# Performance work log

Hardware: AMD Instinct MI355X
Metric: run time of the kernel (lower is better)

## Reference

```python
import jax, jax.numpy as jnp
import numpy as np

L, B, T, D, H, FF = 4, 8, 1024, 256, 8, 1024
DK = D // H
SCALE = 1.0 / np.sqrt(DK)


def _ln(x, g, b, eps=1e-6):
    m = jnp.mean(x, axis=-1, keepdims=True)
    v = jnp.mean(jnp.square(x - m), axis=-1, keepdims=True)
    return (x - m) * jax.lax.rsqrt(v + eps) * g + b


def _l2norm(x, eps=1e-8):
    n = jnp.sqrt(jnp.sum(jnp.square(x), axis=-1, keepdims=True))
    return x / jnp.maximum(n, eps)


def setup_inputs() -> dict:
    key = jax.random.key(0)
    ks = jax.random.split(key, 8)
    s = 0.02
    inp = {
        'x': jax.random.normal(ks[0], (B, T, D), dtype=jnp.float32),
        'padding_mask': jnp.zeros((B, T), dtype=bool),
        'ln1_g': jnp.ones((L, D), jnp.float32), 'ln1_b': jnp.zeros((L, D), jnp.float32),
        'qn_g': jnp.ones((L, D), jnp.float32), 'qn_b': jnp.zeros((L, D), jnp.float32),
        'Wqkv': jax.random.normal(ks[1], (L, 3 * D, D), jnp.float32) * s,
        'bqkv': jnp.zeros((L, 3 * D), jnp.float32),
        'Wo': jax.random.normal(ks[2], (L, D, D), jnp.float32) * s,
        'bo': jnp.zeros((L, D), jnp.float32),
        'ln2_g': jnp.ones((L, D), jnp.float32), 'ln2_b': jnp.zeros((L, D), jnp.float32),
        'W1': jax.random.normal(ks[3], (L, FF, D), jnp.float32) * s,
        'b1': jnp.zeros((L, FF), jnp.float32),
        'W2': jax.random.normal(ks[4], (L, D, FF), jnp.float32) * s,
        'b2': jnp.zeros((L, D), jnp.float32),
        'alpha': jnp.full((L,), 0.1, jnp.float32),
        'beta': jnp.full((L,), 0.1, jnp.float32),
    }
    return inp


def _block(x, pad_mask, p):
    (g1, bb1, qg, qb, wqkv, bqkv, wo, bo, g2, bb2, w1, b1, w2, b2, a, be) = p
    Bn, Tn, Dn = x.shape
    # --- SemiCausalAttention on norm1(x) ---
    xn = _ln(x, g1, bb1)
    h = _ln(xn, qg, qb)                      # q_norm LayerNorm
    qkv = h @ wqkv.T + bqkv                  # [B,T,3D]
    qkv = qkv.reshape(Bn, Tn, 3, H, DK).transpose(2, 0, 3, 1, 4)  # [3,B,H,T,dk]
    Q, K, V = qkv[0], qkv[1], qkv[2]
    Q = _l2norm(Q)
    K = _l2norm(K)
    scores = jnp.einsum('bhtd,bhsd->bhts', Q, K) * SCALE
    scores = jnp.clip(scores, -10.0, 10.0)
    causal = jnp.triu(jnp.ones((Tn, Tn), dtype=bool), k=1)        # True = future
    scores = jnp.where(causal[None, None], -10000.0, scores)
    scores = jnp.where(pad_mask[:, None, None, :], -10000.0, scores)
    attn = jax.nn.softmax(scores, axis=-1)
    ao = jnp.einsum('bhts,bhsd->bhtd', attn, V)                   # [B,H,T,dk]
    ao = ao.transpose(0, 2, 1, 3).reshape(Bn, Tn, Dn)
    attn_out = (ao @ wo.T + bo) * 0.5
    x = x + jnp.tanh(a) * attn_out
    # --- FFN ---
    f = _ln(x, g2, bb2)
    f = jax.nn.gelu(f @ w1.T + b1, approximate=False)
    f = f @ w2.T + b2
    x = x + jnp.tanh(be) * f
    return jnp.clip(x, -100.0, 100.0)


def reference(x, padding_mask, ln1_g, ln1_b, qn_g, qn_b, Wqkv, bqkv, Wo, bo,
              ln2_g, ln2_b, W1, b1, W2, b2, alpha, beta):
    params = (ln1_g, ln1_b, qn_g, qn_b, Wqkv, bqkv, Wo, bo,
              ln2_g, ln2_b, W1, b1, W2, b2, alpha, beta)

    def step(carry, p):
        return _block(carry, padding_mask, p), None

    out, _ = jax.lax.scan(step, x, params)
    return out
```

## Files before the change

### kernel.cpp

```cpp
#include <hip/hip_runtime.h>
#include <hip/hip_bf16.h>
#include <math.h>

#define BB 8
#define TT 1024
#define DD 256
#define HH 8
#define BT 8192

typedef __attribute__((ext_vector_type(4))) float f32x4;
typedef __attribute__((ext_vector_type(16))) float f32x16;
typedef __attribute__((ext_vector_type(8))) short short8;
typedef __attribute__((ext_vector_type(4))) short short4v;
typedef __attribute__((ext_vector_type(8))) __bf16 bf16x8;

__device__ inline float bf2f(short s) {
  unsigned int u = ((unsigned int)(unsigned short)s) << 16;
  return __builtin_bit_cast(float, u);
}
__device__ inline short f2bf(float f) {
  unsigned int u = __builtin_bit_cast(unsigned int, f);
  unsigned int lsb = (u >> 16) & 1u;
  u += 0x7fffu + lsb;
  return (short)(u >> 16);
}
__device__ inline unsigned int cvtpk(float lo, float hi) {
  unsigned int r;
  asm("v_cvt_pk_bf16_f32 %0, %1, %2" : "=v"(r) : "v"(lo), "v"(hi));
  return r;
}

__device__ inline f32x4 mfma16(short8 a, short8 b, f32x4 c) {
  return __builtin_amdgcn_mfma_f32_16x16x32_bf16(
      __builtin_bit_cast(bf16x8, a), __builtin_bit_cast(bf16x8, b), c, 0, 0, 0);
}
__device__ inline f32x16 mfma32(short8 a, short8 b, f32x16 c) {
  return __builtin_amdgcn_mfma_f32_32x32x16_bf16(
      __builtin_bit_cast(bf16x8, a), __builtin_bit_cast(bf16x8, b), c, 0, 0, 0);
}

__device__ inline void gload_lds16(void* lds, const void* g) {
  __builtin_amdgcn_global_load_lds(
      (const __attribute__((address_space(1))) unsigned int*)g,
      (__attribute__((address_space(3))) unsigned int*)lds, 16, 0, 0);
}

__global__ __launch_bounds__(256) void cvt_all(
    const float4* __restrict__ s0, short4v* __restrict__ d0, int n0,
    const float4* __restrict__ s1, short4v* __restrict__ d1, int n1,
    const float4* __restrict__ s2, short4v* __restrict__ d2, int n2,
    const float4* __restrict__ s3, short4v* __restrict__ d3, int n3)
{
  int i = blockIdx.x * 256 + threadIdx.x;
  const float4* s; short4v* d;
  if (i < n0) { s = s0 + i; d = d0 + i; }
  else if ((i -= n0) < n1) { s = s1 + i; d = d1 + i; }
  else if ((i -= n1) < n2) { s = s2 + i; d = d2 + i; }
  else if ((i -= n2) < n3) { s = s3 + i; d = d3 + i; }
  else return;
  float4 v = *s;
  short4v o;
  o[0] = f2bf(v.x); o[1] = f2bf(v.y); o[2] = f2bf(v.z); o[3] = f2bf(v.w);
  *d = o;
}

__global__ __launch_bounds__(256) void ln_kernel(
    const float* __restrict__ Xin,
    const float* __restrict__ g1, const float* __restrict__ b1,
    const float* __restrict__ g2, const float* __restrict__ b2,
    short* __restrict__ out)
{
  const int row = blockIdx.x * 4 + (threadIdx.x >> 6);
  const int lane = threadIdx.x & 63;
  const float4 v = *(const float4*)(Xin + (size_t)row * 256 + lane * 4);
  float y[4] = {v.x, v.y, v.z, v.w};

  float s = y[0] + y[1] + y[2] + y[3];
  #pragma unroll
  for (int m = 32; m >= 1; m >>= 1) s += __shfl_xor(s, m, 64);
  float mean = s * (1.0f / 256.0f);
  float sq = 0.f;
  #pragma unroll
  for (int i = 0; i < 4; ++i) { y[i] -= mean; sq += y[i] * y[i]; }
  #pragma unroll
  for (int m = 32; m >= 1; m >>= 1) sq += __shfl_xor(sq, m, 64);
  float rs = rsqrtf(sq * (1.0f / 256.0f) + 1e-6f);
  #pragma unroll
  for (int i = 0; i < 4; ++i) y[i] = y[i] * rs * g1[lane * 4 + i] + b1[lane * 4 + i];

  float s2 = y[0] + y[1] + y[2] + y[3];
  #pragma unroll
  for (int m = 32; m >= 1; m >>= 1) s2 += __shfl_xor(s2, m, 64);
  float m2 = s2 * (1.0f / 256.0f);
  float sq2 = 0.f;
  #pragma unroll
  for (int i = 0; i < 4; ++i) { y[i] -= m2; sq2 += y[i] * y[i]; }
  #pragma unroll
  for (int m = 32; m >= 1; m >>= 1) sq2 += __shfl_xor(sq2, m, 64);
  float rs2 = rsqrtf(sq2 * (1.0f / 256.0f) + 1e-6f);
  #pragma unroll
  for (int i = 0; i < 4; ++i) y[i] = y[i] * rs2 * g2[lane * 4 + i] + b2[lane * 4 + i];

  #pragma unroll
  for (int i = 0; i < 4; ++i) out[(size_t)row * 256 + lane * 4 + i] = f2bf(y[i]);
}

template<int BN, int EPI>
__global__ __launch_bounds__(256) void gemm_bt(
    const short* __restrict__ A, const short* __restrict__ Bw,
    const float* __restrict__ bias, float* __restrict__ X,
    short* __restrict__ Obf, const float* __restrict__ scale_p,
    int M, int N, int K)
{
  constexpr int MI = (BN == 128) ? 4 : 2;
  __shared__ __align__(16) short A_s[128 * 64];
  __shared__ __align__(16) short B_s[BN * 64];
  const int tid = threadIdx.x;
  const int lane = tid & 63;
  const int w = tid >> 6;
  const int lo4 = lane & 15, hi2 = lane >> 4;
  int wm, wn0;
  if (BN == 128) { wm = (w >> 1) * 64; wn0 = (w & 1) * 64; }
  else           { wm = w * 32;        wn0 = 0; }
  const int bid = blockIdx.x + blockIdx.y * gridDim.x;
  const int nwg = gridDim.x * gridDim.y;
  const int wg = (bid & 7) * (nwg >> 3) + (bid >> 3);
  const int tM = (wg / gridDim.x) * 128, tN = (wg % gridDim.x) * BN;

  f32x4 acc[MI][4];
  #pragma unroll
  for (int i = 0; i < MI; ++i)
    #pragma unroll
    for (int j = 0; j < 4; ++j) acc[i][j] = (f32x4){0.f, 0.f, 0.f, 0.f};

  const int swz = (lo4 & 7) << 3;

  for (int k0 = 0; k0 < K; k0 += 64) {
    #pragma unroll
    for (int ri = 0; ri < 4; ++ri) {
      int o = ri * 2048 + tid * 8;
      int row = o >> 6;
      int col = (o & 63) ^ ((row & 7) << 3);
      gload_lds16(&A_s[ri * 2048 + w * 512], A + (size_t)(tM + row) * K + k0 + col);
    }
    #pragma unroll
    for (int ri = 0; ri < BN / 32; ++ri) {
      int o = ri * 2048 + tid * 8;
      int row = o >> 6;
      int col = (o & 63) ^ ((row & 7) << 3);
      gload_lds16(&B_s[ri * 2048 + w * 512], Bw + (size_t)(tN + row) * K + k0 + col);
    }
    __syncthreads();
    #pragma unroll
    for (int kc = 0; kc < 2; ++kc) {
      short8 af[MI], bfr[4];
      #pragma unroll
      for (int i = 0; i < MI; ++i)
        af[i] = *(const short8*)&A_s[(wm + i * 16 + lo4) * 64 + ((kc * 32 + hi2 * 8) ^ swz)];
      #pragma unroll
      for (int j = 0; j < 4; ++j)
        bfr[j] = *(const short8*)&B_s[(wn0 + j * 16 + lo4) * 64 + ((kc * 32 + hi2 * 8) ^ swz)];
      #pragma unroll
      for (int i = 0; i < MI; ++i)
        #pragma unroll
        for (int j = 0; j < 4; ++j)
          acc[i][j] = mfma16(af[i], bfr[j], acc[i][j]);
    }
    __syncthreads();
  }

  if (EPI == 4) {
    #pragma unroll
    for (int i = 0; i < MI; ++i)
      #pragma unroll
      for (int j = 0; j < 4; ++j)
        #pragma unroll
        for (int r = 0; r < 4; ++r)
          acc[i][j][r] += bias[tN + wn0 + j * 16 + lo4];
    if (tN < 512) {
      const float C2 = 0.25503489702966368f;
      const float sc = (tN < 256) ? C2 : 1.0f;
      #pragma unroll
      for (int i = 0; i < MI; ++i) {
        #pragma unroll
        for (int r = 0; r < 4; ++r) {
          float s01 = acc[i][0][r] * acc[i][0][r] + acc[i][1][r] * acc[i][1][r];
          float s23 = acc[i][2][r] * acc[i][2][r] + acc[i][3][r] * acc[i][3][r];
          #pragma unroll
          for (int m = 1; m <= 8; m <<= 1) {
            s01 += __shfl_xor(s01, m, 64);
            s23 += __shfl_xor(s23, m, 64);
          }
          float n01 = sc / fmaxf(sqrtf(s01), 1e-8f);
          float n23 = sc / fmaxf(sqrtf(s23), 1e-8f);
          acc[i][0][r] *= n01; acc[i][1][r] *= n01;
          acc[i][2][r] *= n23; acc[i][3][r] *= n23;
        }
      }
    }
    #pragma unroll
    for (int i = 0; i < MI; ++i)
      #pragma unroll
      for (int j = 0; j < 4; ++j)
        #pragma unroll
        for (int r = 0; r < 4; ++r) {
          int row = tM + wm + i * 16 + hi2 * 4 + r;
          int col = tN + wn0 + j * 16 + lo4;
          Obf[(size_t)row * N + col] = f2bf(acc[i][j][r]);
        }
    return;
  }

  #pragma unroll
  for (int i = 0; i < MI; ++i) {
    #pragma unroll
    for (int j = 0; j < 4; ++j) {
      #pragma unroll
      for (int r = 0; r < 4; ++r) {
        int row = tM + wm + i * 16 + hi2 * 4 + r;
        int col = tN + wn0 + j * 16 + lo4;
        float v = acc[i][j][r] + bias[col];
        size_t idx = (size_t)row * N + col;
        if (EPI == 2) {
          float gl = 0.5f * v * (1.0f + erff(v * 0.70710678118f));
          Obf[idx] = f2bf(gl);
        } else {
          Obf[idx] = f2bf(v);
        }
      }
    }
  }
}

template<int MODE>
__global__ __launch_bounds__(256) void gemm_ln(
    const short* __restrict__ A, const short* __restrict__ Bw,
    const float* __restrict__ bias, float* __restrict__ X,
    short* __restrict__ Obf, const float* __restrict__ scale_p,
    const float* __restrict__ gA, const float* __restrict__ bA,
    const float* __restrict__ gB, const float* __restrict__ bB,
    int K, int doLN)
{
  __shared__ __align__(16) short A_s[32 * 64];
  __shared__ __align__(16) short B_s[256 * 64];
  __shared__ float Red[2][32][4][2];
  const int tid = threadIdx.x;
  const int lane = tid & 63;
  const int w = tid >> 6;
  const int lo4 = lane & 15, hi2 = lane >> 4;
  const int tM = blockIdx.x * 32;
  const int swz = (lo4 & 7) << 3;

  f32x4 acc[2][4];
  #pragma unroll
  for (int i = 0; i < 2; ++i)
    #pragma unroll
    for (int j = 0; j < 4; ++j) acc[i][j] = (f32x4){0.f, 0.f, 0.f, 0.f};

  for (int k0 = 0; k0 < K; k0 += 64) {
    {
      int o = tid * 8;
      int row = o >> 6;
      int col = (o & 63) ^ ((row & 7) << 3);
      gload_lds16(&A_s[w * 512], A + (size_t)(tM + row) * K + k0 + col);
    }
    #pragma unroll
    for (int ri = 0; ri < 8; ++ri) {
      int o = ri * 2048 + tid * 8;
      int row = o >> 6;
      int col = (o & 63) ^ ((row & 7) << 3);
      gload_lds16(&B_s[ri * 2048 + w * 512], Bw + (size_t)row * K + k0 + col);
    }
    __syncthreads();
    #pragma unroll
    for (int kc = 0; kc < 2; ++kc) {
      short8 af[2], bfr[4];
      #pragma unroll
      for (int i = 0; i < 2; ++i)
        af[i] = *(const short8*)&A_s[(i * 16 + lo4) * 64 + ((kc * 32 + hi2 * 8) ^ swz)];
      #pragma unroll
      for (int j = 0; j < 4; ++j)
        bfr[j] = *(const short8*)&B_s[(w * 64 + j * 16 + lo4) * 64 + ((kc * 32 + hi2 * 8) ^ swz)];
      #pragma unroll
      for (int i = 0; i < 2; ++i)
        #pragma unroll
        for (int j = 0; j < 4; ++j)
          acc[i][j] = mfma16(af[i], bfr[j], acc[i][j]);
    }
    __syncthreads();
  }

  const float ts = tanhf(scale_p[0]);
  float xv[2][4][4];
  #pragma unroll
  for (int i = 0; i < 2; ++i)
    #pragma unroll
    for (int j = 0; j < 4; ++j)
      #pragma unroll
      for (int r = 0; r < 4; ++r) {
        int row = i * 16 + hi2 * 4 + r;
        int col = w * 64 + j * 16 + lo4;
        float v = acc[i][j][r] + bias[col];
        size_t idx = (size_t)(tM + row) * 256 + col;
        float xn;
        if (MODE == 0) {
          xn = X[idx] + ts * 0.5f * v;
        } else {
          xn = X[idx] + ts * v;
          xn = fminf(100.f, fmaxf(-100.f, xn));
        }
        X[idx] = xn;
        xv[i][j][r] = xn;
      }

  if (!doLN) return;

  #pragma unroll
  for (int i = 0; i < 2; ++i)
    #pragma unroll
    for (int r = 0; r < 4; ++r) {
      float s = xv[i][0][r] + xv[i][1][r] + xv[i][2][r] + xv[i][3][r];
      float q = xv[i][0][r] * xv[i][0][r] + xv[i][1][r] * xv[i][1][r]
              + xv[i][2][r] * xv[i][2][r] + xv[i][3][r] * xv[i][3][r];
      #pragma unroll
      for (int m = 1; m <= 8; m <<= 1) { s += __shfl_xor(s, m, 64); q += __shfl_xor(q, m, 64); }
      if (lo4 == 0) { Red[0][i * 16 + hi2 * 4 + r][w][0] = s; Red[0][i * 16 + hi2 * 4 + r][w][1] = q; }
    }
  __syncthreads();
  #pragma unroll
  for (int i = 0; i < 2; ++i)
    #pragma unroll
    for (int r = 0; r < 4; ++r) {
      int row = i * 16 + hi2 * 4 + r;
      float s = Red[0][row][0][0] + Red[0][row][1][0] + Red[0][row][2][0] + Red[0][row][3][0];
      float q = Red[0][row][0][1] + Red[0][row][1][1] + Red[0][row][2][1] + Red[0][row][3][1];
      float mu = s * (1.0f / 256.0f);
      float var = q * (1.0f / 256.0f) - mu * mu;
      float rs = rsqrtf(var + 1e-6f);
      #pragma unroll
      for (int j = 0; j < 4; ++j) {
        int col = w * 64 + j * 16 + lo4;
        xv[i][j][r] = (xv[i][j][r] - mu) * rs * gA[col] + bA[col];
      }
    }

  if (MODE == 1) {
    #pragma unroll
    for (int i = 0; i < 2; ++i)
      #pragma unroll
      for (int r = 0; r < 4; ++r) {
        float s = xv[i][0][r] + xv[i][1][r] + xv[i][2][r] + xv[i][3][r];
        float q = xv[i][0][r] * xv[i][0][r] + xv[i][1][r] * xv[i][1][r]
                + xv[i][2][r] * xv[i][2][r] + xv[i][3][r] * xv[i][3][r];
        #pragma unroll
        for (int m = 1; m <= 8; m <<= 1) { s += __shfl_xor(s, m, 64); q += __shfl_xor(q, m, 64); }
        if (lo4 == 0) { Red[1][i * 16 + hi2 * 4 + r][w][0] = s; Red[1][i * 16 + hi2 * 4 + r][w][1] = q; }
      }
    __syncthreads();
    #pragma unroll
    for (int i = 0; i < 2; ++i)
      #pragma unroll
      for (int r = 0; r < 4; ++r) {
        int row = i * 16 + hi2 * 4 + r;
        float s = Red[1][row][0][0] + Red[1][row][1][0] + Red[1][row][2][0] + Red[1][row][3][0];
        float q = Red[1][row][0][1] + Red[1][row][1][1] + Red[1][row][2][1] + Red[1][row][3][1];
        float mu = s * (1.0f / 256.0f);
        float var = q * (1.0f / 256.0f) - mu * mu;
        float rs = rsqrtf(var + 1e-6f);
        #pragma unroll
        for (int j = 0; j < 4; ++j) {
          int col = w * 64 + j * 16 + lo4;
          xv[i][j][r] = (xv[i][j][r] - mu) * rs * gB[col] + bB[col];
        }
      }
  }

  #pragma unroll
  for (int i = 0; i < 2; ++i)
    #pragma unroll
    for (int j = 0; j < 4; ++j)
      #pragma unroll
      for (int r = 0; r < 4; ++r) {
        int row = i * 16 + hi2 * 4 + r;
        int col = w * 64 + j * 16 + lo4;
        Obf[(size_t)(tM + row) * 256 + col] = f2bf(xv[i][j][r]);
      }
}

__device__ __forceinline__ void pv_acc(const unsigned int* PKO, int half_,
                                       short8 vb, int hi1, f32x16& acc) {
  unsigned int keep0 = hi1 ? PKO[4 * half_ + 2] : PKO[4 * half_ + 0];
  unsigned int keep1 = hi1 ? PKO[4 * half_ + 3] : PKO[4 * half_ + 1];
  unsigned int send0 = hi1 ? PKO[4 * half_ + 0] : PKO[4 * half_ + 2];
  unsigned int send1 = hi1 ? PKO[4 * half_ + 1] : PKO[4 * half_ + 3];
  unsigned int r0 = (unsigned int)__shfl_xor((int)send0, 32, 64);
  unsigned int r1 = (unsigned int)__shfl_xor((int)send1, 32, 64);
  union { unsigned int u[4]; short8 s; } fa;
  fa.u[0] = hi1 ? r0 : keep0;
  fa.u[1] = hi1 ? r1 : keep1;
  fa.u[2] = hi1 ? keep0 : r0;
  fa.u[3] = hi1 ? keep1 : r1;
  acc = mfma32(fa.s, vb, acc);
}

template<bool KG1, bool M0, bool M1>
__device__ __forceinline__ void attn_tile(
    int t, const short* __restrict__ Kbase, const short* __restrict__ Vbase,
    const short8* qb, unsigned int pm0, unsigned int pm1, int lo5, int hi1,
    f32x16& oaccA, f32x16& oaccB, float& rsum)
{
  const short* kp0 = Kbase + (size_t)(t * 64 + lo5) * 768;
  short8 k00 = *(const short8*)(kp0 + hi1 * 8);
  short8 k01 = *(const short8*)(kp0 + 16 + hi1 * 8);
  short8 k10, k11;
  if (KG1) {
    const short* kp1 = Kbase + (size_t)(t * 64 + 32 + lo5) * 768;
    k10 = *(const short8*)(kp1 + hi1 * 8);
    k11 = *(const short8*)(kp1 + 16 + hi1 * 8);
  }
  short8 vb0, vb1, vb2, vb3;
  #pragma unroll
  for (int jj = 0; jj < 8; ++jj) {
    vb0[jj] = Vbase[(size_t)(t * 64 + 0 + hi1 * 8 + jj) * 768 + lo5];
    vb1[jj] = Vbase[(size_t)(t * 64 + 16 + hi1 * 8 + jj) * 768 + lo5];
  }
  if (KG1) {
    #pragma unroll
    for (int jj = 0; jj < 8; ++jj) {
      vb2[jj] = Vbase[(size_t)(t * 64 + 32 + hi1 * 8 + jj) * 768 + lo5];
      vb3[jj] = Vbase[(size_t)(t * 64 + 48 + hi1 * 8 + jj) * 768 + lo5];
    }
  }
  unsigned int pk0[8], pk1[8];
  {
    f32x16 z = (f32x16)0.0f;
    z = mfma32(k00, qb[0], z);
    z = mfma32(k01, qb[1], z);
    float pr[16];
    #pragma unroll
    for (int r = 0; r < 16; ++r) {
      float sv = __builtin_amdgcn_fmed3f(z[r], -14.4269504f, 14.4269504f);
      float pe;
      asm("v_exp_f32 %0, %1" : "=v"(pe) : "v"(sv));
      const int keyrel = (r & 3) + 8 * (r >> 2) + 4 * hi1;
      if (M0) pe = (keyrel > lo5) ? 0.f : pe;
      if (pm0) pe = ((pm0 >> keyrel) & 1u) ? 0.f : pe;
      pr[r] = pe;
      rsum += pe;
    }
    #pragma unroll
    for (int i = 0; i < 8; ++i) pk0[i] = cvtpk(pr[2 * i], pr[2 * i + 1]);
  }
  if (KG1) {
    f32x16 z = (f32x16)0.0f;
    z = mfma32(k10, qb[0], z);
    z = mfma32(k11, qb[1], z);
    float pr[16];
    #pragma unroll
    for (int r = 0; r < 16; ++r) {
      float sv = __builtin_amdgcn_fmed3f(z[r], -14.4269504f, 14.4269504f);
      float pe;
      asm("v_exp_f32 %0, %1" : "=v"(pe) : "v"(sv));
      const int keyrel = (r & 3) + 8 * (r >> 2) + 4 * hi1;
      if (M1) pe = (keyrel > lo5) ? 0.f : pe;
      if (pm1) pe = ((pm1 >> keyrel) & 1u) ? 0.f : pe;
      pr[r] = pe;
      rsum += pe;
    }
    #pragma unroll
    for (int i = 0; i < 8; ++i) pk1[i] = cvtpk(pr[2 * i], pr[2 * i + 1]);
  }
  pv_acc(pk0, 0, vb0, hi1, oaccA);
  pv_acc(pk0, 1, vb1, hi1, oaccB);
  if (KG1) {
    pv_acc(pk1, 0, vb2, hi1, oaccA);
    pv_acc(pk1, 1, vb3, hi1, oaccB);
  }
}

__global__ __launch_bounds__(256, 2) void attn_kernel(
    const short* __restrict__ qkv, const unsigned char* __restrict__ pad,
    short* __restrict__ ao)
{
  __shared__ float Red[2][17][64];
  const int tid = threadIdx.x, lane = tid & 63, w = tid >> 6;
  const int lo5 = lane & 31, hi1 = lane >> 5;
  const int bid = blockIdx.x;
  const int b = bid & 7;
  const int h = (bid >> 3) & 7;
  const int bj = bid >> 6;
  const int p = w >> 1;
  const int half = w & 1;
  const int j = p ? (31 - bj) : bj;
  const size_t rowbase = (size_t)b * TT;
  const int qrow = j * 32 + lo5;
  const int ntile = (j >> 1) + 1;

  const short* Kbase = qkv + rowbase * 768 + 256 + h * 32;
  const short* Vbase = qkv + rowbase * 768 + 512 + h * 32;

  const ulonglong2 pv = *(const ulonglong2*)(pad + rowbase + lane * 16);
  const unsigned long long anyp = __ballot((pv.x | pv.y) != 0ull);

  short8 qb[2];
  #pragma unroll
  for (int c2 = 0; c2 < 2; ++c2)
    qb[c2] = *(const short8*)(qkv + (rowbase + qrow) * 768 + h * 32 + c2 * 16 + hi1 * 8);

  f32x16 oaccA = (f32x16)0.0f;
  f32x16 oaccB = (f32x16)0.0f;
  float rsum = 0.f;

  for (int t = half; t < ntile; t += 2) {
    unsigned long long pm = 0;
    if ((anyp >> (4 * t)) & 0xFull)
      pm = __ballot(pad[rowbase + t * 64 + lane] != 0);
    unsigned int pm0 = (unsigned int)pm, pm1 = (unsigned int)(pm >> 32);
    if (t + 1 < ntile)
      attn_tile<true, false, false>(t, Kbase, Vbase, qb, pm0, pm1, lo5, hi1, oaccA, oaccB, rsum);
    else if (j & 1)
      attn_tile<true, false, true>(t, Kbase, Vbase, qb, pm0, pm1, lo5, hi1, oaccA, oaccB, rsum);
    else
      attn_tile<false, true, false>(t, Kbase, Vbase, qb, pm0, pm1, lo5, hi1, oaccA, oaccB, rsum);
  }

  if (half) {
    #pragma unroll
    for (int r = 0; r < 16; ++r) Red[p][r][lane] = oaccA[r] + oaccB[r];
    Red[p][16][lane] = rsum;
  }
  __syncthreads();
  if (!half) {
    #pragma unroll
    for (int r = 0; r < 16; ++r) oaccA[r] += oaccB[r] + Red[p][r][lane];
    rsum += Red[p][16][lane];
    rsum += __shfl_xor(rsum, 32, 64);
    float rinv = 1.0f / fmaxf(rsum, 1e-30f);
    #pragma unroll
    for (int r = 0; r < 16; ++r) {
      int ql = (r & 3) + 8 * (r >> 2) + 4 * hi1;
      float riv = __shfl(rinv, ql, 64);
      int qg = j * 32 + ql;
      ao[(rowbase + qg) * 256 + h * 32 + lo5] = f2bf(oaccA[r] * riv);
    }
  }
}

extern "C" void kernel_launch(void* const* d_in, const int* in_sizes, int n_in,
                              void* d_out, int out_size, void* d_ws, size_t ws_size,
                              hipStream_t stream) {
  const float* x_in  = (const float*)d_in[0];
  const unsigned char* pad = (const unsigned char*)d_in[1];
  const float* ln1_g = (const float*)d_in[2];
  const float* ln1_b = (const float*)d_in[3];
  const float* qn_g  = (const float*)d_in[4];
  const float* qn_b  = (const float*)d_in[5];
  const float* Wqkv  = (const float*)d_in[6];
  const float* bqkv  = (const float*)d_in[7];
  const float* Wo    = (const float*)d_in[8];
  const float* bo    = (const float*)d_in[9];
  const float* ln2_g = (const float*)d_in[10];
  const float* ln2_b = (const float*)d_in[11];
  const float* W1    = (const float*)d_in[12];
  const float* b1    = (const float*)d_in[13];
  const float* W2    = (const float*)d_in[14];
  const float* b2    = (const float*)d_in[15];
  const float* alpha = (const float*)d_in[16];
  const float* beta  = (const float*)d_in[17];

  char* ws = (char*)d_ws;
  size_t off = 0;
  short* wqkv_bf = (short*)(ws + off); off += (size_t)4 * 768 * 256 * 2;
  short* wo_bf   = (short*)(ws + off); off += (size_t)4 * 256 * 256 * 2;
  short* w1_bf   = (short*)(ws + off); off += (size_t)4 * 1024 * 256 * 2;
  short* w2_bf   = (short*)(ws + off); off += (size_t)4 * 256 * 1024 * 2;
  short* h_bf    = (short*)(ws + off); off += (size_t)BT * 256 * 2;
  short* qkv_bf  = (short*)(ws + off); off += (size_t)BT * 768 * 2;
  short* ao_bf   = (short*)(ws + off); off += (size_t)BT * 256 * 2;
  short* g_bf    = (short*)(ws + off); off += (size_t)BT * 1024 * 2;

  float* X = (float*)d_out;

  hipMemcpyAsync(d_out, x_in, (size_t)BT * DD * 4, hipMemcpyDeviceToDevice, stream);
  cvt_all<<<3072, 256, 0, stream>>>(
      (const float4*)Wqkv, (short4v*)wqkv_bf, 4 * 768 * 256 / 4,
      (const float4*)Wo,   (short4v*)wo_bf,   4 * 256 * 256 / 4,
      (const float4*)W1,   (short4v*)w1_bf,   4 * 1024 * 256 / 4,
      (const float4*)W2,   (short4v*)w2_bf,   4 * 256 * 1024 / 4);

  ln_kernel<<<2048, 256, 0, stream>>>(X, ln1_g, ln1_b, qn_g, qn_b, h_bf);

  for (int l = 0; l < 4; ++l) {
    gemm_bt<128, 4><<<dim3(6, 64), 256, 0, stream>>>(h_bf, wqkv_bf + (size_t)l * 768 * 256,
                                                     bqkv + l * 768, nullptr, qkv_bf, nullptr,
                                                     8192, 768, 256);
    attn_kernel<<<1024, 256, 0, stream>>>(qkv_bf, pad, ao_bf);
    gemm_ln<0><<<256, 256, 0, stream>>>(ao_bf, wo_bf + (size_t)l * 256 * 256,
                                        bo + l * 256, X, h_bf, alpha + l,
                                        ln2_g + l * 256, ln2_b + l * 256,
                                        nullptr, nullptr, 256, 1);
    gemm_bt<128, 2><<<dim3(8, 64), 256, 0, stream>>>(h_bf, w1_bf + (size_t)l * 1024 * 256,
                                                     b1 + l * 1024, nullptr, g_bf, nullptr,
                                                     8192, 1024, 256);
    const int nl = (l < 3) ? (l + 1) : 0;
    gemm_ln<1><<<256, 256, 0, stream>>>(g_bf, w2_bf + (size_t)l * 256 * 1024,
                                        b2 + l * 256, X, h_bf, beta + l,
                                        ln1_g + nl * 256, ln1_b + nl * 256,
                                        qn_g + nl * 256, qn_b + nl * 256,
                                        1024, (l < 3) ? 1 : 0);
  }
}
```

Baseline: 380.5 us.

## Pre-transpose V for vectorized attention loads and deepen GEMM K-tiles

Adds a transpose kernel that writes V per (batch, head) as a contiguous d-major buffer. The attention kernel can then fetch V fragments with 16-byte vector loads instead of strided scalar gathers. Separately, both GEMM kernels now stage 128-wide K tiles instead of 64, halving loop iterations and barriers. The cost is an extra launch plus the V buffer round trip, and up to 64KB of LDS in gemm_ln, which may reduce occupancy.

```diff
diff --git a/kernel.cpp b/kernel.cpp
--- a/kernel.cpp
+++ b/kernel.cpp
@@ -105,6 +105,35 @@
   for (int i = 0; i < 4; ++i) out[(size_t)row * 256 + lane * 4 + i] = f2bf(y[i]);
 }
 
+__global__ __launch_bounds__(256) void vtr_kernel(
+    const short* __restrict__ qkv, short* __restrict__ vT)
+{
+  __shared__ short T_s[32][264];
+  const int tid = threadIdx.x;
+  const int bh = blockIdx.x >> 2;
+  const int tc = blockIdx.x & 3;
+  const int b = bh >> 3, h = bh & 7;
+  const int t = tc * 256 + tid;
+  const short* src = qkv + ((size_t)b * TT + t) * 768 + 512 + h * 32;
+  short8 v0 = *(const short8*)(src);
+  short8 v1 = *(const short8*)(src + 8);
+  short8 v2 = *(const short8*)(src + 16);
+  short8 v3 = *(const short8*)(src + 24);
+  #pragma unroll
+  for (int d = 0; d < 8; ++d) {
+    T_s[d][tid] = v0[d];
+    T_s[d + 8][tid] = v1[d];
+    T_s[d + 16][tid] = v2[d];
+    T_s[d + 24][tid] = v3[d];
+  }
+  __syncthreads();
+  const int d = tid >> 3, toff = (tid & 7) * 32;
+  short* dst = vT + ((size_t)bh * 32 + d) * 1024 + tc * 256 + toff;
+  #pragma unroll
+  for (int s = 0; s < 4; ++s)
+    *(short8*)(dst + s * 8) = *(const short8*)&T_s[d][toff + s * 8];
+}
+
 template<int BN, int EPI>
 __global__ __launch_bounds__(256) void gemm_bt(
     const short* __restrict__ A, const short* __restrict__ Bw,
@@ -113,8 +142,8 @@
     int M, int N, int K)
 {
   constexpr int MI = (BN == 128) ? 4 : 2;
-  __shared__ __align__(16) short A_s[128 * 64];
-  __shared__ __align__(16) short B_s[BN * 64];
+  __shared__ __align__(16) short A_s[128 * 128];
+  __shared__ __align__(16) short B_s[BN * 128];
   const int tid = threadIdx.x;
   const int lane = tid & 63;
   const int w = tid >> 6;
@@ -133,33 +162,36 @@
     #pragma unroll
     for (int j = 0; j < 4; ++j) acc[i][j] = (f32x4){0.f, 0.f, 0.f, 0.f};
 
-  const int swz = (lo4 & 7) << 3;
-
-  for (int k0 = 0; k0 < K; k0 += 64) {
-    #pragma unroll
-    for (int ri = 0; ri < 4; ++ri) {
+  const int rswzA = ((wm + lo4) & 7) << 3;
+  for (int k0 = 0; k0 < K; k0 += 128) {
+    #pragma unroll
+    for (int ri = 0; ri < 8; ++ri) {
       int o = ri * 2048 + tid * 8;
-      int row = o >> 6;
-      int col = (o & 63) ^ ((row & 7) << 3);
+      int row = o >> 7;
+      int col = (o & 127) ^ ((row & 7) << 3);
       gload_lds16(&A_s[ri * 2048 + w * 512], A + (size_t)(tM + row) * K + k0 + col);
     }
     #pragma unroll
-    for (int ri = 0; ri < BN / 32; ++ri) {
+    for (int ri = 0; ri < BN / 16; ++ri) {
       int o = ri * 2048 + tid * 8;
-      int row = o >> 6;
-      int col = (o & 63) ^ ((row & 7) << 3);
+      int row = o >> 7;
+      int col = (o & 127) ^ ((row & 7) << 3);
       gload_lds16(&B_s[ri * 2048 + w * 512], Bw + (size_t)(tN + row) * K + k0 + col);
     }
     __syncthreads();
     #pragma unroll
-    for (int kc = 0; kc < 2; ++kc) {
+    for (int kc = 0; kc < 4; ++kc) {
       short8 af[MI], bfr[4];
       #pragma unroll
-      for (int i = 0; i < MI; ++i)
-        af[i] = *(const short8*)&A_s[(wm + i * 16 + lo4) * 64 + ((kc * 32 + hi2 * 8) ^ swz)];
-      #pragma unroll
-      for (int j = 0; j < 4; ++j)
-        bfr[j] = *(const short8*)&B_s[(wn0 + j * 16 + lo4) * 64 + ((kc * 32 + hi2 * 8) ^ swz)];
+      for (int i = 0; i < MI; ++i) {
+        int row = wm + i * 16 + lo4;
+        af[i] = *(const short8*)&A_s[row * 128 + ((kc * 32 + hi2 * 8) ^ ((row & 7) << 3))];
+      }
+      #pragma unroll
+      for (int j = 0; j < 4; ++j) {
+        int row = wn0 + j * 16 + lo4;
+        bfr[j] = *(const short8*)&B_s[row * 128 + ((kc * 32 + hi2 * 8) ^ ((row & 7) << 3))];
+      }
       #pragma unroll
       for (int i = 0; i < MI; ++i)
         #pragma unroll
@@ -168,6 +200,7 @@
     }
     __syncthreads();
   }
+  (void)rswzA;
 
   if (EPI == 4) {
     #pragma unroll
@@ -241,15 +274,14 @@
     const float* __restrict__ gB, const float* __restrict__ bB,
     int K, int doLN)
 {
-  __shared__ __align__(16) short A_s[32 * 64];
-  __shared__ __align__(16) short B_s[256 * 64];
+  __shared__ __align__(16) short A_s[32 * 128];
+  __shared__ __align__(16) short B_s[256 * 128];
   __shared__ float Red[2][32][4][2];
   const int tid = threadIdx.x;
   const int lane = tid & 63;
   const int w = tid >> 6;
   const int lo4 = lane & 15, hi2 = lane >> 4;
   const int tM = blockIdx.x * 32;
-  const int swz = (lo4 & 7) << 3;
 
   f32x4 acc[2][4];
   #pragma unroll
@@ -257,30 +289,35 @@
     #pragma unroll
     for (int j = 0; j < 4; ++j) acc[i][j] = (f32x4){0.f, 0.f, 0.f, 0.f};
 
-  for (int k0 = 0; k0 < K; k0 += 64) {
-    {
-      int o = tid * 8;
-      int row = o >> 6;
-      int col = (o & 63) ^ ((row & 7) << 3);
-      gload_lds16(&A_s[w * 512], A + (size_t)(tM + row) * K + k0 + col);
-    }
-    #pragma unroll
-    for (int ri = 0; ri < 8; ++ri) {
+  for (int k0 = 0; k0 < K; k0 += 128) {
+    #pragma unroll
+    for (int ri = 0; ri < 2; ++ri) {
       int o = ri * 2048 + tid * 8;
-      int row = o >> 6;
-      int col = (o & 63) ^ ((row & 7) << 3);
+      int row = o >> 7;
+      int col = (o & 127) ^ ((row & 7) << 3);
+      gload_lds16(&A_s[ri * 2048 + w * 512], A + (size_t)(tM + row) * K + k0 + col);
+    }
+    #pragma unroll
+    for (int ri = 0; ri < 16; ++ri) {
+      int o = ri * 2048 + tid * 8;
+      int row = o >> 7;
+      int col = (o & 127) ^ ((row & 7) << 3);
       gload_lds16(&B_s[ri * 2048 + w * 512], Bw + (size_t)row * K + k0 + col);
     }
     __syncthreads();
     #pragma unroll
-    for (int kc = 0; kc < 2; ++kc) {
+    for (int kc = 0; kc < 4; ++kc) {
       short8 af[2], bfr[4];
       #pragma unroll
-      for (int i = 0; i < 2; ++i)
-        af[i] = *(const short8*)&A_s[(i * 16 + lo4) * 64 + ((kc * 32 + hi2 * 8) ^ swz)];
-      #pragma unroll
-      for (int j = 0; j < 4; ++j)
-        bfr[j] = *(const short8*)&B_s[(w * 64 + j * 16 + lo4) * 64 + ((kc * 32 + hi2 * 8) ^ swz)];
+      for (int i = 0; i < 2; ++i) {
+        int row = i * 16 + lo4;
+        af[i] = *(const short8*)&A_s[row * 128 + ((kc * 32 + hi2 * 8) ^ ((row & 7) << 3))];
+      }
+      #pragma unroll
+      for (int j = 0; j < 4; ++j) {
+        int row = w * 64 + j * 16 + lo4;
+        bfr[j] = *(const short8*)&B_s[row * 128 + ((kc * 32 + hi2 * 8) ^ ((row & 7) << 3))];
+      }
       #pragma unroll
       for (int i = 0; i < 2; ++i)
         #pragma unroll
@@ -405,7 +442,7 @@
 
 template<bool KG1, bool M0, bool M1>
 __device__ __forceinline__ void attn_tile(
-    int t, const short* __restrict__ Kbase, const short* __restrict__ Vbase,
+    int t, const short* __restrict__ Kbase, const short* __restrict__ VTl,
     const short8* qb, unsigned int pm0, unsigned int pm1, int lo5, int hi1,
     f32x16& oaccA, f32x16& oaccB, float& rsum)
 {
@@ -418,18 +455,13 @@
     k10 = *(const short8*)(kp1 + hi1 * 8);
     k11 = *(const short8*)(kp1 + 16 + hi1 * 8);
   }
-  short8 vb0, vb1, vb2, vb3;
-  #pragma unroll
-  for (int jj = 0; jj < 8; ++jj) {
-    vb0[jj] = Vbase[(size_t)(t * 64 + 0 + hi1 * 8 + jj) * 768 + lo5];
-    vb1[jj] = Vbase[(size_t)(t * 64 + 16 + hi1 * 8 + jj) * 768 + lo5];
-  }
+  const short* vp = VTl + t * 64 + hi1 * 8;
+  short8 vb0 = *(const short8*)(vp);
+  short8 vb1 = *(const short8*)(vp + 16);
+  short8 vb2, vb3;
   if (KG1) {
-    #pragma unroll
-    for (int jj = 0; jj < 8; ++jj) {
-      vb2[jj] = Vbase[(size_t)(t * 64 + 32 + hi1 * 8 + jj) * 768 + lo5];
-      vb3[jj] = Vbase[(size_t)(t * 64 + 48 + hi1 * 8 + jj) * 768 + lo5];
-    }
+    vb2 = *(const short8*)(vp + 32);
+    vb3 = *(const short8*)(vp + 48);
   }
   unsigned int pk0[8], pk1[8];
   {
@@ -479,8 +511,8 @@
 }
 
 __global__ __launch_bounds__(256, 2) void attn_kernel(
-    const short* __restrict__ qkv, const unsigned char* __restrict__ pad,
-    short* __restrict__ ao)
+    const short* __restrict__ qkv, const short* __restrict__ vT,
+    const unsigned char* __restrict__ pad, short* __restrict__ ao)
 {
   __shared__ float Red[2][17][64];
   const int tid = threadIdx.x, lane = tid & 63, w = tid >> 6;
@@ -497,7 +529,7 @@
   const int ntile = (j >> 1) + 1;
 
   const short* Kbase = qkv + rowbase * 768 + 256 + h * 32;
-  const short* Vbase = qkv + rowbase * 768 + 512 + h * 32;
+  const short* VTl = vT + ((size_t)(b * 8 + h) * 32 + lo5) * 1024;
 
   const ulonglong2 pv = *(const ulonglong2*)(pad + rowbase + lane * 16);
   const unsigned long long anyp = __ballot((pv.x | pv.y) != 0ull);
@@ -517,11 +549,11 @@
       pm = __ballot(pad[rowbase + t * 64 + lane] != 0);
     unsigned int pm0 = (unsigned int)pm, pm1 = (unsigned int)(pm >> 32);
     if (t + 1 < ntile)
-      attn_tile<true, false, false>(t, Kbase, Vbase, qb, pm0, pm1, lo5, hi1, oaccA, oaccB, rsum);
+      attn_tile<true, false, false>(t, Kbase, VTl, qb, pm0, pm1, lo5, hi1, oaccA, oaccB, rsum);
     else if (j & 1)
-      attn_tile<true, false, true>(t, Kbase, Vbase, qb, pm0, pm1, lo5, hi1, oaccA, oaccB, rsum);
+      attn_tile<true, false, true>(t, Kbase, VTl, qb, pm0, pm1, lo5, hi1, oaccA, oaccB, rsum);
     else
-      attn_tile<false, true, false>(t, Kbase, Vbase, qb, pm0, pm1, lo5, hi1, oaccA, oaccB, rsum);
+      attn_tile<false, true, false>(t, Kbase, VTl, qb, pm0, pm1, lo5, hi1, oaccA, oaccB, rsum);
   }
 
   if (half) {
@@ -578,6 +610,7 @@
   short* qkv_bf  = (short*)(ws + off); off += (size_t)BT * 768 * 2;
   short* ao_bf   = (short*)(ws + off); off += (size_t)BT * 256 * 2;
   short* g_bf    = (short*)(ws + off); off += (size_t)BT * 1024 * 2;
+  short* vT_bf   = (short*)(ws + off); off += (size_t)BT * 256 * 2;
 
   float* X = (float*)d_out;
 
@@ -594,7 +627,8 @@
     gemm_bt<128, 4><<<dim3(6, 64), 256, 0, stream>>>(h_bf, wqkv_bf + (size_t)l * 768 * 256,
                                                      bqkv + l * 768, nullptr, qkv_bf, nullptr,
                                                      8192, 768, 256);
-    attn_kernel<<<1024, 256, 0, stream>>>(qkv_bf, pad, ao_bf);
+    vtr_kernel<<<256, 256, 0, stream>>>(qkv_bf, vT_bf);
+    attn_kernel<<<1024, 256, 0, stream>>>(qkv_bf, vT_bf, pad, ao_bf);
     gemm_ln<0><<<256, 256, 0, stream>>>(ao_bf, wo_bf + (size_t)l * 256 * 256,
                                         bo + l * 256, X, h_bf, alpha + l,
                                         ln2_g + l * 256, ln2_b + l * 256,
```

After: 380.7 us. No clear change (+0.1%).
